# Kernel tuning notes

Measured on AMD Instinct MI355X. Metric: run time of the kernel, lower is better.

## Reference

```python
import jax, jax.numpy as jnp
import numpy as np

B, S, N, D, H = 4, 2048, 2048, 1024, 16
HD = D // H  # 64
EPS = 1e-5


def layer_norm(x, w, b):
    m = x.mean(axis=-1, keepdims=True)
    v = ((x - m) ** 2).mean(axis=-1, keepdims=True)
    return (x - m) / jnp.sqrt(v + EPS) * w + b


def setup_inputs() -> dict:
    key = jax.random.key(0)
    ks = jax.random.split(key, 4)
    x_q = jax.random.normal(ks[0], (B, S, D), dtype=jnp.float32)
    x_k = jax.random.normal(ks[1], (B, N, HD), dtype=jnp.float32)
    x_v = jax.random.normal(ks[2], (B, N, HD), dtype=jnp.float32)
    # learned params
    qn_w = jnp.ones((HD,), jnp.float32)
    qn_b = jnp.zeros((HD,), jnp.float32)
    kn_w = jnp.ones((HD,), jnp.float32)
    kn_b = jnp.zeros((HD,), jnp.float32)
    n_w = jnp.ones((D,), jnp.float32)
    n_b = jnp.zeros((D,), jnp.float32)
    # xavier-uniform proj weight (D, D), no bias (proj_bias=False)
    limit = np.sqrt(6.0 / (D + D))
    proj_w = jax.random.uniform(ks[3], (D, D), jnp.float32, -limit, limit)
    return {"x_q": x_q, "x_k": x_k, "x_v": x_v,
            "qn_w": qn_w, "qn_b": qn_b, "kn_w": kn_w, "kn_b": kn_b,
            "n_w": n_w, "n_b": n_b, "proj_w": proj_w}


def reference(x_q, x_k, x_v, qn_w, qn_b, kn_w, kn_b, n_w, n_b, proj_w):
    scale = HD ** -0.5
    # faithful to torch: q.reshape(B, H, -1, head_dim) -- NO transpose before reshape
    q = x_q.reshape(B, H, S, HD)
    q = layer_norm(q, qn_w, qn_b)
    k = layer_norm(x_k, kn_w, kn_b)
    q = q * scale
    attn = jnp.einsum('bhsd,bnd->bhsn', q, k)  # (B,H,S,N) shared K across heads
    attn = jax.nn.softmax(attn, axis=-1)
    x = jnp.einsum('bhsn,bnd->bhsd', attn, x_v)  # shared V across heads
    x = jnp.transpose(x, (0, 2, 1, 3)).reshape(B, S, D)
    x = layer_norm(x, n_w, n_b)
    x = x @ proj_w.T  # nn.Linear: x W^T
    return x
```

## Files before the change

kernel.cpp:

```cpp
#include <hip/hip_runtime.h>

#define B_ 4
#define S_ 2048
#define N_ 2048
#define H_ 16
#define D_ 1024

typedef short s4v __attribute__((ext_vector_type(4)));
typedef short s8v __attribute__((ext_vector_type(8)));
typedef float f4v __attribute__((ext_vector_type(4)));

__device__ __forceinline__ float bf2f(short s) {
  unsigned u = ((unsigned)(unsigned short)s) << 16;
  float f; __builtin_memcpy(&f, &u, 4); return f;
}
__device__ __forceinline__ short f2bf(float f) {
  unsigned u; __builtin_memcpy(&u, &f, 4);
  u += 0x7fffu + ((u >> 16) & 1u);
  return (short)(u >> 16);
}
__device__ __forceinline__ unsigned pack2bf(float a, float b) {
  unsigned ua, ub;
  __builtin_memcpy(&ua, &a, 4);
  __builtin_memcpy(&ub, &b, 4);
  return __builtin_amdgcn_perm(ub + 0x8000u, ua + 0x8000u, 0x07060302u);
}
__device__ __forceinline__ unsigned pk2(float a, float b) {
  unsigned ua, ub;
  __builtin_memcpy(&ua, &a, 4);
  __builtin_memcpy(&ub, &b, 4);
  return __builtin_amdgcn_perm(ub, ua, 0x07060302u);
}
__device__ __forceinline__ s8v load8f32(const float* p) {
  const f4v* q = (const f4v*)p;
  f4v a = q[0], b = q[1];
  union { s8v v; unsigned u[4]; } o;
  o.u[0] = pack2bf(a[0], a[1]); o.u[1] = pack2bf(a[2], a[3]);
  o.u[2] = pack2bf(b[0], b[1]); o.u[3] = pack2bf(b[2], b[3]);
  return o.v;
}
__device__ __forceinline__ void gld16(const char* g, char* l) {
  __builtin_amdgcn_global_load_lds(
      (const __attribute__((address_space(1))) unsigned*)g,
      (__attribute__((address_space(3))) unsigned*)l, 16, 0, 0);
}

__global__ __launch_bounds__(256) void prep_kernel(
    const float* __restrict__ xk, const float* __restrict__ knw,
    const float* __restrict__ knb, short* __restrict__ kws,
    const float* __restrict__ xv, short* __restrict__ vtp) {
  __shared__ __align__(16) short vstage[4][2048];
  int blk = blockIdx.x;
  if (blk < 2048) {
    int gid = blk * 256 + threadIdx.x;
    int row = gid >> 6, lane = gid & 63;
    float v = xk[(size_t)row * 64 + lane];
    float s = v;
    #pragma unroll
    for (int mm = 1; mm < 64; mm <<= 1) s += __shfl_xor(s, mm, 64);
    float mean = s * 0.015625f;
    float d = v - mean;
    float vs = d * d;
    #pragma unroll
    for (int mm = 1; mm < 64; mm <<= 1) vs += __shfl_xor(vs, mm, 64);
    float rstd = rsqrtf(vs * 0.015625f + 1e-5f);
    kws[(size_t)row * 72 + lane] = f2bf(d * rstd * knw[lane] + knb[lane]);
  } else {
    int wave = threadIdx.x >> 6, lane = threadIdx.x & 63;
    int u = (blk - 2048) * 4 + wave;
    int b = u >> 6, nb = u & 63;
    int r = lane >> 1, dh = lane & 1;
    const float* src = xv + ((size_t)(b * N_ + nb * 32 + r)) * 64 + dh * 32;
    int qq = (r & 15) >> 2;
    int slot = ((r >> 4) << 2) + (r & 3);
    short* wbase = &vstage[wave][0];
    #pragma unroll
    for (int jj = 0; jj < 32; jj += 4) {
      f4v f = *(const f4v*)(src + jj);
      #pragma unroll
      for (int e = 0; e < 4; e++) {
        int d = dh * 32 + jj + e;
        wbase[d * 32 + qq * 8 + slot] = f2bf(f[e]);
      }
    }
    __syncthreads();
    s8v* dst = (s8v*)(vtp + (size_t)u * 2560 + lane * 40);
    const s8v* sp = (const s8v*)(wbase + lane * 32);
    dst[0] = sp[0]; dst[1] = sp[1]; dst[2] = sp[2]; dst[3] = sp[3];
  }
}

__global__ __launch_bounds__(256, 4) void flash_kernel(
    const float* __restrict__ xq, const float* __restrict__ qnw,
    const float* __restrict__ qnb, const short* __restrict__ kws,
    const short* __restrict__ vtp, short* __restrict__ aout) {
  __shared__ __align__(16) union {
    char qs[128 * 144];
    struct { char k[2][9216]; char v[2][10240]; } kv;
  } lds;
  int blk = blockIdx.x;
  int sblk = blk & 15, bh = blk >> 4, b = bh >> 4;
  int t = threadIdx.x, wave = t >> 6, lane = t & 63;
  int m = lane & 15, q = lane >> 4;
  const float QSCALE = 0.125f * 1.4426950408889634f;

  const char* kb = (const char*)kws + (size_t)b * N_ * 144;
  const char* vb = (const char*)vtp + (size_t)b * 64 * 5120;

  gld16(vb + t * 16,        lds.kv.v[0] + t * 16);
  gld16(vb + 4096 + t * 16, lds.kv.v[0] + 4096 + t * 16);
  if (t < 128) gld16(vb + 8192 + t * 16, lds.kv.v[0] + 8192 + t * 16);

  {
    int r = t >> 1, half = t & 1;
    const float* qr = xq + ((size_t)bh * S_ + sblk * 128 + r) * 64 + half * 32;
    f4v f[8];
    float s = 0.f, ss = 0.f;
    #pragma unroll
    for (int i = 0; i < 8; i++) {
      f[i] = *(const f4v*)(qr + i * 4);
      s += (f[i][0] + f[i][1]) + (f[i][2] + f[i][3]);
      ss += (f[i][0] * f[i][0] + f[i][1] * f[i][1]) + (f[i][2] * f[i][2] + f[i][3] * f[i][3]);
    }
    s += __shfl_xor(s, 1, 64);
    ss += __shfl_xor(ss, 1, 64);
    float mean = s * 0.015625f;
    float rstd = rsqrtf(ss * 0.015625f - mean * mean + 1e-5f);
    #pragma unroll
    for (int i = 0; i < 4; i++) {
      float y[8];
      #pragma unroll
      for (int e = 0; e < 4; e++) {
        int gi = half * 32 + i * 8;
        y[e]     = ((f[2 * i][e]     - mean) * rstd * qnw[gi + e]     + qnb[gi + e])     * QSCALE;
        y[4 + e] = ((f[2 * i + 1][e] - mean) * rstd * qnw[gi + 4 + e] + qnb[gi + 4 + e]) * QSCALE;
      }
      union { s8v v; unsigned u[4]; } o8;
      #pragma unroll
      for (int e = 0; e < 4; e++) o8.u[e] = pack2bf(y[2 * e], y[2 * e + 1]);
      *(s8v*)(lds.qs + r * 144 + half * 64 + i * 16) = o8.v;
    }
  }
  __syncthreads();

  s8v qlo[2], qhi[2];
  #pragma unroll
  for (int mt = 0; mt < 2; mt++) {
    const char* qrow = lds.qs + (wave * 32 + mt * 16 + m) * 144;
    qlo[mt] = *(const s8v*)(qrow + q * 16);
    qhi[mt] = *(const s8v*)(qrow + 64 + q * 16);
  }
  __syncthreads();

  gld16(kb + t * 16,        lds.kv.k[0] + t * 16);
  gld16(kb + 4096 + t * 16, lds.kv.k[0] + 4096 + t * 16);
  if (t < 64) gld16(kb + 8192 + t * 16, lds.kv.k[0] + 8192 + t * 16);
  __syncthreads();

  f4v zero4 = {0.f, 0.f, 0.f, 0.f};
  f4v o[2][4], lacc[2];
  #pragma unroll
  for (int mt = 0; mt < 2; mt++) {
    lacc[mt] = zero4;
    #pragma unroll
    for (int tt = 0; tt < 4; tt++) o[mt][tt] = zero4;
  }
  s8v ones;
  #pragma unroll
  for (int e = 0; e < 8; e++) ones[e] = (short)0x3F80;

  for (int it = 0; it < 32; ++it) {
    int cur = it & 1;
    if (it < 31) {
      const char* kg = kb + (size_t)(it + 1) * 9216;
      const char* vg = vb + (size_t)(it + 1) * 10240;
      char* kd = lds.kv.k[cur ^ 1];
      char* vd = lds.kv.v[cur ^ 1];
      gld16(kg + t * 16,        kd + t * 16);
      gld16(kg + 4096 + t * 16, kd + 4096 + t * 16);
      if (t < 64) gld16(kg + 8192 + t * 16, kd + 8192 + t * 16);
      gld16(vg + t * 16,        vd + t * 16);
      gld16(vg + 4096 + t * 16, vd + 4096 + t * 16);
      if (t < 128) gld16(vg + 8192 + t * 16, vd + 8192 + t * 16);
    }
    const char* kc = lds.kv.k[cur];
    const char* vc = lds.kv.v[cur];

    #pragma unroll
    for (int g = 0; g < 2; g++) {
      s8v a0lo = *(const s8v*)(kc + (g * 32 + m) * 144 + q * 16);
      s8v a0hi = *(const s8v*)(kc + (g * 32 + m) * 144 + 64 + q * 16);
      s8v a1lo = *(const s8v*)(kc + (g * 32 + 16 + m) * 144 + q * 16);
      s8v a1hi = *(const s8v*)(kc + (g * 32 + 16 + m) * 144 + 64 + q * 16);
      s8v vf[4];
      #pragma unroll
      for (int tt = 0; tt < 4; tt++)
        vf[tt] = *(const s8v*)(vc + g * 5120 + (tt * 16 + m) * 80 + q * 16);

      #pragma unroll
      for (int mt = 0; mt < 2; mt++) {
        f4v s0 = zero4, s1 = zero4;
        s0 = __builtin_amdgcn_mfma_f32_16x16x32_bf16(a0lo, qlo[mt], s0, 0, 0, 0);
        s0 = __builtin_amdgcn_mfma_f32_16x16x32_bf16(a0hi, qhi[mt], s0, 0, 0, 0);
        s1 = __builtin_amdgcn_mfma_f32_16x16x32_bf16(a1lo, qlo[mt], s1, 0, 0, 0);
        s1 = __builtin_amdgcn_mfma_f32_16x16x32_bf16(a1hi, qhi[mt], s1, 0, 0, 0);
        float p[8];
        #pragma unroll
        for (int i = 0; i < 4; i++) {
          p[i]     = __builtin_amdgcn_exp2f(s0[i]);
          p[4 + i] = __builtin_amdgcn_exp2f(s1[i]);
        }
        union { s8v v; unsigned u[4]; } pa;
        #pragma unroll
        for (int i = 0; i < 4; i++) pa.u[i] = pk2(p[2 * i], p[2 * i + 1]);
        lacc[mt] = __builtin_amdgcn_mfma_f32_16x16x32_bf16(pa.v, ones, lacc[mt], 0, 0, 0);
        #pragma unroll
        for (int tt = 0; tt < 4; tt++)
          o[mt][tt] = __builtin_amdgcn_mfma_f32_16x16x32_bf16(pa.v, vf[tt], o[mt][tt], 0, 0, 0);
      }
    }
    __syncthreads();
  }

  #pragma unroll
  for (int mt = 0; mt < 2; mt++) {
    #pragma unroll
    for (int i = 0; i < 4; i++) {
      float inv = __builtin_amdgcn_rcpf(lacc[mt][i]);
      int srow = sblk * 128 + wave * 32 + mt * 16 + q * 4 + i;
      size_t orow = ((size_t)b * S_ + srow) * D_ + (size_t)(bh & 15) * 64;
      #pragma unroll
      for (int tt = 0; tt < 4; tt++)
        aout[orow + tt * 16 + m] = f2bf(o[mt][tt][i] * inv);
    }
  }
}

__global__ __launch_bounds__(256) void ln_d_kernel(
    const short* __restrict__ x, const float* __restrict__ w,
    const float* __restrict__ bb, short* __restrict__ y) {
  int row = blockIdx.x * 4 + (threadIdx.x >> 6);
  int lane = threadIdx.x & 63;
  const short* xr = x + (size_t)row * D_ + lane * 16;
  s8v v0 = *(const s8v*)xr;
  s8v v1 = *(const s8v*)(xr + 8);
  float f[16];
  #pragma unroll
  for (int e = 0; e < 8; e++) { f[e] = bf2f(v0[e]); f[8 + e] = bf2f(v1[e]); }
  float s = 0.f, ss = 0.f;
  #pragma unroll
  for (int e = 0; e < 16; e++) { s += f[e]; ss += f[e] * f[e]; }
  #pragma unroll
  for (int mm = 1; mm < 64; mm <<= 1) {
    s += __shfl_xor(s, mm, 64);
    ss += __shfl_xor(ss, mm, 64);
  }
  float mean = s * (1.0f / 1024.0f);
  float rstd = rsqrtf(ss * (1.0f / 1024.0f) - mean * mean + 1e-5f);
  const float* wp = w + lane * 16;
  const float* bp = bb + lane * 16;
  union { s8v v[2]; short sh[16]; } o;
  #pragma unroll
  for (int e = 0; e < 16; e++)
    o.sh[e] = f2bf((f[e] - mean) * rstd * wp[e] + bp[e]);
  short* yr = y + (size_t)row * D_ + lane * 16;
  *(s8v*)yr = o.v[0];
  *(s8v*)(yr + 8) = o.v[1];
}

__global__ __launch_bounds__(256) void proj_gemm(
    const short* __restrict__ A, const float* __restrict__ Bw,
    float* __restrict__ C) {
  __shared__ __align__(16) char la[128 * 80];
  __shared__ __align__(16) char lb[128 * 80];
  int bm = (blockIdx.x >> 3) * 128;
  int bn = (blockIdx.x & 7) * 128;
  int wave = threadIdx.x >> 6, lane = threadIdx.x & 63;
  int m = lane & 15, q = lane >> 4;
  int wm = (wave & 1) * 64, wn = (wave >> 1) * 64;
  f4v zero4 = {0.f, 0.f, 0.f, 0.f};
  f4v acc[4][4];
  #pragma unroll
  for (int i = 0; i < 4; i++)
    #pragma unroll
    for (int j = 0; j < 4; j++) acc[i][j] = zero4;
  int sr = threadIdx.x >> 1, sh = (threadIdx.x & 1) * 16;
  for (int k0 = 0; k0 < 1024; k0 += 32) {
    s8v a0 = *(const s8v*)(A + (size_t)(bm + sr) * 1024 + k0 + sh);
    s8v a1 = *(const s8v*)(A + (size_t)(bm + sr) * 1024 + k0 + sh + 8);
    s8v b0 = load8f32(Bw + (size_t)(bn + sr) * 1024 + k0 + sh);
    s8v b1 = load8f32(Bw + (size_t)(bn + sr) * 1024 + k0 + sh + 8);
    __syncthreads();
    *(s8v*)(la + sr * 80 + sh * 2) = a0;
    *(s8v*)(la + sr * 80 + sh * 2 + 16) = a1;
    *(s8v*)(lb + sr * 80 + sh * 2) = b0;
    *(s8v*)(lb + sr * 80 + sh * 2 + 16) = b1;
    __syncthreads();
    s8v af[4], bfv[4];
    #pragma unroll
    for (int i = 0; i < 4; i++) af[i] = *(const s8v*)(la + (wm + i * 16 + m) * 80 + q * 16);
    #pragma unroll
    for (int j = 0; j < 4; j++) bfv[j] = *(const s8v*)(lb + (wn + j * 16 + m) * 80 + q * 16);
    #pragma unroll
    for (int i = 0; i < 4; i++)
      #pragma unroll
      for (int j = 0; j < 4; j++)
        acc[i][j] = __builtin_amdgcn_mfma_f32_16x16x32_bf16(af[i], bfv[j], acc[i][j], 0, 0, 0);
  }
  #pragma unroll
  for (int i = 0; i < 4; i++)
    #pragma unroll
    for (int j = 0; j < 4; j++)
      #pragma unroll
      for (int r = 0; r < 4; r++) {
        int row = bm + wm + i * 16 + q * 4 + r;
        int col = bn + wn + j * 16 + m;
        C[(size_t)row * 1024 + col] = acc[i][j][r];
      }
}

extern "C" void kernel_launch(void* const* d_in, const int* in_sizes, int n_in,
                              void* d_out, int out_size, void* d_ws, size_t ws_size,
                              hipStream_t stream) {
  const float* xq  = (const float*)d_in[0];
  const float* xk  = (const float*)d_in[1];
  const float* xv  = (const float*)d_in[2];
  const float* qnw = (const float*)d_in[3];
  const float* qnb = (const float*)d_in[4];
  const float* knw = (const float*)d_in[5];
  const float* knb = (const float*)d_in[6];
  const float* nw  = (const float*)d_in[7];
  const float* nb  = (const float*)d_in[8];
  const float* pw  = (const float*)d_in[9];
  float* out = (float*)d_out;

  short* kws = (short*)d_ws;
  short* vtp = (short*)((char*)d_ws + 0x120000);
  short* yws = (short*)d_ws;
  short* aout = (short*)d_out;

  prep_kernel<<<2112, 256, 0, stream>>>(xk, knw, knb, kws, xv, vtp);
  flash_kernel<<<1024, 256, 0, stream>>>(xq, qnw, qnb, kws, vtp, aout);
  ln_d_kernel<<<B_ * S_ / 4, 256, 0, stream>>>(aout, nw, nb, yws);
  proj_gemm<<<512, 256, 0, stream>>>(yws, pw, out);
}
```

Before: 226.6 us.

## Double-buffer projection GEMM with async global-to-LDS loads, XOR swizzle and BK=64

Restructures the projection GEMM main loop to use two LDS buffers, so the next K tile's loads are issued before the MFMAs on the current tile and only one barrier is needed per iteration. The A tile is fetched with direct global-to-LDS 16-byte loads into an XOR-swizzled layout that replaces the padded rows. The K step grows from 32 to 64, workgroups are remapped for L2 locality, and launch bounds request two blocks per CU. The cost is 64KB of LDS per block and more register pressure, and the GEMM is only one part of the pipeline.

```diff
diff --git a/kernel.cpp b/kernel.cpp
--- a/kernel.cpp
+++ b/kernel.cpp
@@ -268,45 +268,90 @@
   *(s8v*)(yr + 8) = o.v[1];
 }
 
-__global__ __launch_bounds__(256) void proj_gemm(
+__global__ __launch_bounds__(256, 2) void proj_gemm(
     const short* __restrict__ A, const float* __restrict__ Bw,
     float* __restrict__ C) {
-  __shared__ __align__(16) char la[128 * 80];
-  __shared__ __align__(16) char lb[128 * 80];
-  int bm = (blockIdx.x >> 3) * 128;
-  int bn = (blockIdx.x & 7) * 128;
-  int wave = threadIdx.x >> 6, lane = threadIdx.x & 63;
+  __shared__ __align__(16) char la[2][16384];
+  __shared__ __align__(16) char lb[2][16384];
+  int wg = (blockIdx.x & 7) * 64 + (blockIdx.x >> 3);
+  int bm = (wg >> 3) * 128;
+  int bn = (wg & 7) * 128;
+  int t = threadIdx.x, wave = t >> 6, lane = t & 63;
   int m = lane & 15, q = lane >> 4;
   int wm = (wave & 1) * 64, wn = (wave >> 1) * 64;
+
+  int arow0 = t >> 3, au = t & 7;
+  const char* abase = (const char*)(A + (size_t)bm * 1024);
+  int brow = t >> 1, bu0 = (t & 1) * 4;
+  const float* bwbase = Bw + (size_t)(bn + brow) * 1024;
+  char* lbrow0 = lb[0] + brow * 128;
+  char* lbrow1 = lb[1] + brow * 128;
+
   f4v zero4 = {0.f, 0.f, 0.f, 0.f};
   f4v acc[4][4];
   #pragma unroll
   for (int i = 0; i < 4; i++)
     #pragma unroll
     for (int j = 0; j < 4; j++) acc[i][j] = zero4;
-  int sr = threadIdx.x >> 1, sh = (threadIdx.x & 1) * 16;
-  for (int k0 = 0; k0 < 1024; k0 += 32) {
-    s8v a0 = *(const s8v*)(A + (size_t)(bm + sr) * 1024 + k0 + sh);
-    s8v a1 = *(const s8v*)(A + (size_t)(bm + sr) * 1024 + k0 + sh + 8);
-    s8v b0 = load8f32(Bw + (size_t)(bn + sr) * 1024 + k0 + sh);
-    s8v b1 = load8f32(Bw + (size_t)(bn + sr) * 1024 + k0 + sh + 8);
+
+  #pragma unroll
+  for (int c = 0; c < 4; c++) {
+    int row = c * 32 + arow0;
+    gld16(abase + (size_t)row * 2048 + (size_t)(au ^ (row & 7)) * 16,
+          la[0] + c * 4096 + t * 16);
+  }
+  #pragma unroll
+  for (int j = 0; j < 4; j++) {
+    int u = bu0 + j;
+    s8v bv = load8f32(bwbase + u * 8);
+    *(s8v*)(lbrow0 + ((u ^ (brow & 7)) * 16)) = bv;
+  }
+  __syncthreads();
+
+  for (int it = 0; it < 16; ++it) {
+    int cur = it & 1;
+    if (it < 15) {
+      int k0 = (it + 1) * 64;
+      char* ad = la[cur ^ 1];
+      char* bd = (cur ^ 1) ? lbrow1 : lbrow0;
+      #pragma unroll
+      for (int c = 0; c < 4; c++) {
+        int row = c * 32 + arow0;
+        gld16(abase + (size_t)row * 2048 + (size_t)k0 * 2 +
+                  (size_t)(au ^ (row & 7)) * 16,
+              ad + c * 4096 + t * 16);
+      }
+      #pragma unroll
+      for (int j = 0; j < 4; j++) {
+        int u = bu0 + j;
+        s8v bv = load8f32(bwbase + k0 + u * 8);
+        *(s8v*)(bd + ((u ^ (brow & 7)) * 16)) = bv;
+      }
+    }
+    const char* lac = la[cur];
+    const char* lbc = lb[cur];
+    #pragma unroll
+    for (int kh = 0; kh < 2; kh++) {
+      s8v af[4], bfv[4];
+      #pragma unroll
+      for (int i = 0; i < 4; i++) {
+        int r = wm + i * 16 + m;
+        af[i] = *(const s8v*)(lac + r * 128 + (((kh * 4 + q) ^ (r & 7)) * 16));
+      }
+      #pragma unroll
+      for (int j = 0; j < 4; j++) {
+        int r = wn + j * 16 + m;
+        bfv[j] = *(const s8v*)(lbc + r * 128 + (((kh * 4 + q) ^ (r & 7)) * 16));
+      }
+      #pragma unroll
+      for (int i = 0; i < 4; i++)
+        #pragma unroll
+        for (int j = 0; j < 4; j++)
+          acc[i][j] = __builtin_amdgcn_mfma_f32_16x16x32_bf16(af[i], bfv[j], acc[i][j], 0, 0, 0);
+    }
     __syncthreads();
-    *(s8v*)(la + sr * 80 + sh * 2) = a0;
-    *(s8v*)(la + sr * 80 + sh * 2 + 16) = a1;
-    *(s8v*)(lb + sr * 80 + sh * 2) = b0;
-    *(s8v*)(lb + sr * 80 + sh * 2 + 16) = b1;
-    __syncthreads();
-    s8v af[4], bfv[4];
-    #pragma unroll
-    for (int i = 0; i < 4; i++) af[i] = *(const s8v*)(la + (wm + i * 16 + m) * 80 + q * 16);
-    #pragma unroll
-    for (int j = 0; j < 4; j++) bfv[j] = *(const s8v*)(lb + (wn + j * 16 + m) * 80 + q * 16);
-    #pragma unroll
-    for (int i = 0; i < 4; i++)
-      #pragma unroll
-      for (int j = 0; j < 4; j++)
-        acc[i][j] = __builtin_amdgcn_mfma_f32_16x16x32_bf16(af[i], bfv[j], acc[i][j], 0, 0, 0);
-  }
+  }
+
   #pragma unroll
   for (int i = 0; i < 4; i++)
     #pragma unroll
```

Measured after the change: 219.1 us. 1.03x faster.
